# Kernel optimization log

Hardware: AMD Instinct MI355X
Metric: run time of the kernel (lower is better)

Reference implementation:

```python
import jax, jax.numpy as jnp
import numpy as np

# dims: L blocks, S cur_seq, M memory_len, B batch, D embed, H heads, IN input_dim
L, S, M, B, D, H, IN = 4, 512, 512, 8, 1024, 16, 128
HD = D // H
GRU_BIAS = 2.0  # config['gru_bias']


def _ln(x, s, b, eps=1e-5):
    mu = x.mean(-1, keepdims=True)
    var = ((x - mu) ** 2).mean(-1, keepdims=True)
    return (x - mu) * jax.lax.rsqrt(var + eps) * s + b


def _pos_emb(full_seq, dim):
    # SinusoidalPE: freqs = arange(0, dim, 2.0); inv = 10000**(-freqs/dim); seq descending
    freqs = jnp.arange(0, dim, 2.0)
    inv = 10000.0 ** (-freqs / dim)
    seq = jnp.arange(full_seq - 1, -1, -1.0)
    ang = seq[:, None] * inv[None, :]
    return jnp.concatenate([jnp.sin(ang), jnp.cos(ang)], axis=-1)  # (F, dim)


def _rel_shift(x):
    # x: (q, k, b, h) -> Transformer-XL relative shift
    q, k, b, h = x.shape
    xp = jnp.pad(x, ((0, 0), (1, 0), (0, 0), (0, 0)))
    return xp.reshape(k + 1, q, b, h)[1:].reshape(q, k, b, h)


def _gru(x, y, Wr, Ur, Wz, Uz, Wg, Ug):
    r = jax.nn.sigmoid(y @ Wr + x @ Ur)
    z = jax.nn.sigmoid(y @ Wz + x @ Uz - GRU_BIAS)
    hcand = jnp.tanh(y @ Wg + (r * x) @ Ug)
    return (1.0 - z) * x + z * hcand


def setup_inputs() -> dict:
    key = jax.random.key(0)
    ks = iter(jax.random.split(key, 64))

    def mat(*shape):
        return jax.random.normal(next(ks), shape, jnp.float32) * (shape[-2] ** -0.5)

    return dict(
        h=jax.random.normal(next(ks), (B, S, IN), jnp.float32),
        memory=jnp.zeros((L, M, B, D), jnp.float32),
        We=mat(IN, D), be=jnp.zeros((D,), jnp.float32),
        ln1_s=jnp.ones((L, D), jnp.float32), ln1_b=jnp.zeros((L, D), jnp.float32),
        ln2_s=jnp.ones((L, D), jnp.float32), ln2_b=jnp.zeros((L, D), jnp.float32),
        Wq=mat(L, D, D), bq=jnp.zeros((L, D), jnp.float32),
        Wk=mat(L, D, D), bk=jnp.zeros((L, D), jnp.float32),
        Wv=mat(L, D, D), bv=jnp.zeros((L, D), jnp.float32),
        Wr=mat(L, D, D), br=jnp.zeros((L, D), jnp.float32),
        Wo=mat(L, D, D), bo=jnp.zeros((L, D), jnp.float32),
        u=jax.random.normal(next(ks), (L, H, HD), jnp.float32) * 0.02,
        vb=jax.random.normal(next(ks), (L, H, HD), jnp.float32) * 0.02,
        gWr=mat(L, 2, D, D), gUr=mat(L, 2, D, D),
        gWz=mat(L, 2, D, D), gUz=mat(L, 2, D, D),
        gWg=mat(L, 2, D, D), gUg=mat(L, 2, D, D),
        fW1=mat(L, D, 4 * D), fb1=jnp.zeros((L, 4 * D), jnp.float32),
        fW2=mat(L, 4 * D, D), fb2=jnp.zeros((L, D), jnp.float32),
    )


def reference(h, memory, We, be, ln1_s, ln1_b, ln2_s, ln2_b,
              Wq, bq, Wk, bk, Wv, bv, Wr, br, Wo, bo, u, vb,
              gWr, gUr, gWz, gUz, gWg, gUg, fW1, fb1, fW2, fb2):
    x = jnp.transpose(h, (1, 0, 2))                      # (S, B, IN)
    x = jax.nn.gelu(x @ We + be, approximate=False)      # (S, B, D)
    F = S + M
    pos = _pos_emb(F, D)                                 # (F, D)
    mask = jnp.triu(jnp.ones((S, F), bool), k=1 + M)     # (S, F)
    scale = HD ** -0.5
    out = x
    for i in range(L):
        full = jnp.concatenate([memory[i], out], axis=0)  # (F, B, D)
        qn = _ln(out, ln1_s[i], ln1_b[i])
        kn = _ln(full, ln1_s[i], ln1_b[i])
        q = (qn @ Wq[i] + bq[i]).reshape(S, B, H, HD)
        k = (kn @ Wk[i] + bk[i]).reshape(F, B, H, HD)
        v = (kn @ Wv[i] + bv[i]).reshape(F, B, H, HD)
        r = (pos @ Wr[i] + br[i]).reshape(F, H, HD)
        content = jnp.einsum('ibhd,jbhd->ijbh', q + u[i], k)
        position = _rel_shift(jnp.einsum('ibhd,jhd->ijbh', q + vb[i], r))
        attn = (content + position) * scale               # (S, F, B, H)
        attn = jnp.where(mask[:, :, None, None], -1e30, attn)
        a = jax.nn.softmax(attn, axis=1)
        y = jnp.einsum('ijbh,jbhd->ibhd', a, v).reshape(S, B, D) @ Wo[i] + bo[i]
        y = jax.nn.gelu(y, approximate=False)
        out1 = _gru(out, y, gWr[i, 0], gUr[i, 0], gWz[i, 0], gUz[i, 0], gWg[i, 0], gUg[i, 0])
        e = _ln(out1, ln2_s[i], ln2_b[i])
        e = jax.nn.gelu(e @ fW1[i] + fb1[i], approximate=False)
        e = jax.nn.gelu(e @ fW2[i] + fb2[i], approximate=False)
        out = _gru(out1, e, gWr[i, 1], gUr[i, 1], gWz[i, 1], gUz[i, 1], gWg[i, 1], gUg[i, 1])
    return jnp.transpose(out, (1, 0, 2))                  # (B, S, D)
```

## Files before the change

### kernel.cpp

```cpp
#include <hip/hip_runtime.h>

typedef unsigned short u16;
typedef unsigned long long u64;
typedef __attribute__((ext_vector_type(8))) short bf16x8;
typedef __attribute__((ext_vector_type(4))) float f32x4;

#define DEVI __device__ __forceinline__

DEVI u16 f2b(float f) {
  unsigned u = __float_as_uint(f);
  u += 0x7fffu + ((u >> 16) & 1u);
  return (u16)(u >> 16);
}
DEVI float b2f(u16 v) { return __uint_as_float((unsigned)v << 16); }
DEVI float tanh_f(float x) {
  float xc = fminf(fmaxf(x, -15.f), 15.f);
  float e = __expf(2.f * xc);
  return (e - 1.f) / (e + 1.f);
}
DEVI float gelu_f(float x) {
  float u = 0.7978845608028654f * x * (1.f + 0.044715f * x * x);
  return 0.5f * x * (1.f + tanh_f(u));
}
DEVI float sigm_f(float x) { return 1.f / (1.f + __expf(-x)); }

DEVI void gload16(const void* g, void* l) {
  __builtin_amdgcn_global_load_lds((__attribute__((address_space(1))) void*)g,
                                   (__attribute__((address_space(3))) void*)l, 16, 0, 0);
}

template <int BN>
__global__ __launch_bounds__(256) void gemm_bt(
    const u16* __restrict__ A, const u16* __restrict__ Bt,
    const float* __restrict__ bias, const float* __restrict__ bias2,
    float* __restrict__ C32, u16* __restrict__ C16, u16* __restrict__ C16b,
    int M, int N, int K, int ldA, int ldB, int ldC,
    long long sA, long long sBb, long long sBh, long long sC, int nH, int flags)
{
  constexpr int NF = BN / 32;
  __shared__ __align__(16) u16 Sm[2][(128 + BN) * 64];
  const int z = blockIdx.z;
  const int zb = z / nH, zh = z - zb * nH;
  A  += (long long)z * sA;
  Bt += (long long)zb * sBb + (long long)zh * sBh;
  const long long cOff = (long long)z * sC;
  const int m0 = blockIdx.x * 128, n0 = blockIdx.y * BN;
  const int t = threadIdx.x, lane = t & 63;
  const int wm = ((t >> 7) & 1) * 64, wn = ((t >> 6) & 1) * (BN / 2);

  f32x4 acc[4][NF];
#pragma unroll
  for (int i = 0; i < 4; ++i)
#pragma unroll
    for (int j = 0; j < NF; ++j) { f32x4 zz = {0.f, 0.f, 0.f, 0.f}; acc[i][j] = zz; }

  auto stage = [&](int buf, int k0) {
#pragma unroll
    for (int r = 0; r < 4; ++r) {
      const int c = r * 256 + t;
      const int row = c >> 3;
      const int col = (c & 7) << 3;
      int ga = m0 + row; if (ga >= M) ga = M - 1;
      gload16(A + (long long)ga * ldA + (k0 + col),
              &Sm[buf][(size_t)(r * 256 + (t & 192)) * 8]);
    }
#pragma unroll
    for (int r = 0; r < BN / 32; ++r) {
      const int c = r * 256 + t;
      const int row = c >> 3;
      const int col = (c & 7) << 3;
      int gb = n0 + row; if (gb >= N) gb = N - 1;
      gload16(Bt + (long long)gb * ldB + (k0 + col),
              &Sm[buf][(size_t)(1024 + r * 256 + (t & 192)) * 8]);
    }
  };

  auto compute = [&](int buf) {
    const u16* As = &Sm[buf][0];
    const u16* Bs = &Sm[buf][128 * 64];
#pragma unroll
    for (int ks = 0; ks < 2; ++ks) {
      const int ko = ks * 32 + ((lane >> 4) << 3);
      bf16x8 af[4], bfv[NF];
#pragma unroll
      for (int i = 0; i < 4; ++i)
        af[i] = *(const bf16x8*)&As[(wm + i * 16 + (lane & 15)) * 64 + ko];
#pragma unroll
      for (int i = 0; i < NF; ++i)
        bfv[i] = *(const bf16x8*)&Bs[(wn + i * 16 + (lane & 15)) * 64 + ko];
#pragma unroll
      for (int mi = 0; mi < 4; ++mi)
#pragma unroll
        for (int ni = 0; ni < NF; ++ni)
          acc[mi][ni] = __builtin_amdgcn_mfma_f32_16x16x32_bf16(af[mi], bfv[ni], acc[mi][ni], 0, 0, 0);
    }
  };

  stage(0, 0);
  __syncthreads();
  int cur = 0;
  for (int k0 = 64; k0 < K; k0 += 64) {
    stage(cur ^ 1, k0);
    compute(cur);
    __syncthreads();
    cur ^= 1;
  }
  compute(cur);

  const int cb = n0 + wn + (lane & 15);
  const int rb = m0 + wm + ((lane >> 4) << 2);
#pragma unroll
  for (int ni = 0; ni < NF; ++ni) {
    const int col = cb + ni * 16;
    if (col >= N) continue;
    float bv = 0.f;
    if (flags & 2) bv = ((flags & 128) && zh) ? bias2[col] : bias[col];
#pragma unroll
    for (int mi = 0; mi < 4; ++mi) {
#pragma unroll
      for (int q = 0; q < 4; ++q) {
        const int row = rb + mi * 16 + q;
        if (row >= M) continue;
        float x = acc[mi][ni][q] + bv;
        if (flags & 1) x = gelu_f(x);
        if (flags & 64) {
          const long long o = ((long long)((row & 7) * 16 + (col >> 6)) * ldC + (row >> 3)) * 64 + (col & 63);
          C16[o] = f2b(x);
          C16b[o] = f2b(x + bias2[col]);
        } else if (flags & 128) {
          if (zh == 0) {
            const long long o = ((long long)((row & 7) * 16 + (col >> 6)) * ldC + (row >> 3)) * 64 + (col & 63);
            C16[o] = f2b(x);
          } else {
            C16b[(long long)row * 1024 + col] = f2b(x);
          }
        } else {
          long long o;
          if (flags & 16)
            o = ((long long)((row & 7) * 16 + (col >> 6)) * ldC + (row >> 3)) * 64 + (col & 63);
          else if (flags & 32)
            o = ((long long)(col >> 6) * 1024 + row) * 64 + (col & 63);
          else
            o = cOff + (long long)row * ldC + col;
          if (flags & 4) C32[o] = x;
          if (flags & 8) C16[o] = f2b(x);
        }
      }
    }
  }
}

__global__ __launch_bounds__(256) void fused_attn(
    const u16* __restrict__ Qu,
    const u16* __restrict__ Qv,
    const u16* __restrict__ Kb,
    const u16* __restrict__ Vt,
    const u16* __restrict__ Rh,
    u16* __restrict__ Y)
{
  constexpr int F = 1024;
  constexpr float KSC = 0.1803368801111244f;
  const int bid = blockIdx.x;
  const int wk = (bid & 7) * 128 + (bid >> 3);
  const int i0 = (wk & 7) * 64;
  const int bh = wk >> 3;
  const int h = bh & 15;

  __shared__ __align__(16) u16 Ks[2][64 * 64];
  __shared__ __align__(16) u16 Vs[2][64 * 64];
  __shared__ __align__(16) u16 Rs[2][64 * 64];
  __shared__ __align__(8) u16 PBT[2][64 * 68];
  __shared__ __align__(16) u16 Ps[4][16][72];

  const int t = threadIdx.x;
  const int lane = t & 63;
  const int wq = t >> 6;
  const int l15 = lane & 15, lhi = lane >> 4;

  const u16* QUg = Qu + ((size_t)bh * 512 + i0) * 64;
  const u16* QVg = Qv + ((size_t)bh * 512 + i0) * 64;
  const u16* Kg = Kb + (size_t)bh * F * 64;
  const u16* Vg = Vt + (size_t)bh * 64 * F;
  const u16* Rg = Rh + (size_t)h * F * 64;

  bf16x8 au[2], av[2];
#pragma unroll
  for (int ks = 0; ks < 2; ++ks) {
    const int arow = wq * 16 + l15;
    au[ks] = *(const bf16x8*)(QUg + arow * 64 + ks * 32 + lhi * 8);
    av[ks] = *(const bf16x8*)(QVg + arow * 64 + ks * 32 + lhi * 8);
  }

  auto stageT = [&](const u16* g, u16* dst) {
#pragma unroll
    for (int rnd = 0; rnd < 2; ++rnd) {
      const int idx = rnd * 256 + t;
      const int row = idx >> 3;
      const int gs = (idx & 7) ^ (row & 7);
      gload16(g + row * 64 + gs * 8, dst + (size_t)(rnd * 256 + (t & 192)) * 8);
    }
  };
  auto stageVf = [&](int j0, u16* dst) {
#pragma unroll
    for (int rnd = 0; rnd < 2; ++rnd) {
      const int idx = rnd * 256 + t;
      const int row = idx >> 3;
      const int gs = (idx & 7) ^ (row & 7);
      gload16(Vg + (size_t)row * F + j0 + gs * 8, dst + (size_t)(rnd * 256 + (t & 192)) * 8);
    }
  };

  const int nT = i0 / 64 + 9;

  stageT(Kg, Ks[0]);
  stageVf(0, Vs[0]);
  stageT(Rg + (size_t)(512 - i0) * 64, Rs[0]);
  stageT(Rg + (size_t)(448 - i0) * 64, Rs[1]);
  __syncthreads();
  {
    f32x4 pb0[4];
#pragma unroll
    for (int i = 0; i < 4; ++i) { f32x4 zz = {0.f, 0.f, 0.f, 0.f}; pb0[i] = zz; }
    __builtin_amdgcn_s_setprio(1);
#pragma unroll
    for (int ks = 0; ks < 2; ++ks)
#pragma unroll
      for (int ni = 0; ni < 4; ++ni) {
        const int brow = ni * 16 + l15;
        const bf16x8 br_ = *(const bf16x8*)&Rs[1][brow * 64 + (((ks * 4 + lhi) ^ (brow & 7)) << 3)];
        pb0[ni] = __builtin_amdgcn_mfma_f32_16x16x32_bf16(av[ks], br_, pb0[ni], 0, 0, 0);
      }
    __builtin_amdgcn_s_setprio(0);
#pragma unroll
    for (int ni = 0; ni < 4; ++ni) {
      u64 w = (u64)f2b(pb0[ni][0]) | ((u64)f2b(pb0[ni][1]) << 16) |
              ((u64)f2b(pb0[ni][2]) << 32) | ((u64)f2b(pb0[ni][3]) << 48);
      *(u64*)&PBT[0][(size_t)(ni * 16 + l15) * 68 + wq * 16 + lhi * 4] = w;
    }
  }
  __syncthreads();

  f32x4 Oacc[4];
#pragma unroll
  for (int i = 0; i < 4; ++i) { f32x4 zz = {0.f, 0.f, 0.f, 0.f}; Oacc[i] = zz; }
  float mrow[4] = {-3.0e38f, -3.0e38f, -3.0e38f, -3.0e38f};
  float lrow[4] = {0.f, 0.f, 0.f, 0.f};

  for (int st = 0; st < nT; ++st) {
    const int b = st & 1;
    const bool lastT = (st == nT - 1);

    if (!lastT) {
      const int j1 = (st + 1) * 64;
      stageT(Kg + (size_t)j1 * 64, Ks[b ^ 1]);
      stageVf(j1, Vs[b ^ 1]);
      if (st + 1 < nT - 1)
        stageT(Rg + (size_t)(j1 - i0 + 512) * 64, Rs[b ^ 1]);
    }

    f32x4 cacc[4], pbh[4];
#pragma unroll
    for (int i = 0; i < 4; ++i) {
      f32x4 zz = {0.f, 0.f, 0.f, 0.f};
      cacc[i] = zz; pbh[i] = zz;
    }
    __builtin_amdgcn_s_setprio(1);
#pragma unroll
    for (int ks = 0; ks < 2; ++ks) {
#pragma unroll
      for (int ni = 0; ni < 4; ++ni) {
        const int brow = ni * 16 + l15;
        const bf16x8 bk_ = *(const bf16x8*)&Ks[b][brow * 64 + (((ks * 4 + lhi) ^ (brow & 7)) << 3)];
        cacc[ni] = __builtin_amdgcn_mfma_f32_16x16x32_bf16(au[ks], bk_, cacc[ni], 0, 0, 0);
      }
      if (!lastT) {
#pragma unroll
        for (int ni = 0; ni < 4; ++ni) {
          const int brow = ni * 16 + l15;
          const bf16x8 br_ = *(const bf16x8*)&Rs[b][brow * 64 + (((ks * 4 + lhi) ^ (brow & 7)) << 3)];
          pbh[ni] = __builtin_amdgcn_mfma_f32_16x16x32_bf16(av[ks], br_, pbh[ni], 0, 0, 0);
        }
      }
    }
    __builtin_amdgcn_s_setprio(0);

    if (!lastT) {
#pragma unroll
      for (int ni = 0; ni < 4; ++ni) {
        u64 w = (u64)f2b(pbh[ni][0]) | ((u64)f2b(pbh[ni][1]) << 16) |
                ((u64)f2b(pbh[ni][2]) << 32) | ((u64)f2b(pbh[ni][3]) << 48);
        *(u64*)&PBT[(st + 1) & 1][(size_t)(ni * 16 + l15) * 68 + wq * 16 + lhi * 4] = w;
      }
    }

    const u16* pbLo = &PBT[st & 1][0];
    const u16* pbHi = &PBT[(st + 1) & 1][0];
    float sc[4][4];
#pragma unroll
    for (int ni = 0; ni < 4; ++ni) {
      const int dj = ni * 16 + l15;
#pragma unroll
      for (int qq = 0; qq < 4; ++qq) {
        const int di = wq * 16 + lhi * 4 + qq;
        const int cc = dj - di + 63;
        const float pb = b2f((cc < 64) ? pbLo[(size_t)cc * 68 + di]
                                       : pbHi[(size_t)(cc - 64) * 68 + di]);
        float s = (cacc[ni][qq] + pb) * KSC;
        if (lastT && dj > di) s = -1e30f;
        sc[ni][qq] = s;
      }
    }

    float nm[4], esc[4];
#pragma unroll
    for (int qq = 0; qq < 4; ++qq) {
      float r = fmaxf(fmaxf(sc[0][qq], sc[1][qq]), fmaxf(sc[2][qq], sc[3][qq]));
      r = fmaxf(r, __shfl_xor(r, 1));
      r = fmaxf(r, __shfl_xor(r, 2));
      r = fmaxf(r, __shfl_xor(r, 4));
      r = fmaxf(r, __shfl_xor(r, 8));
      nm[qq] = fmaxf(mrow[qq], r);
      esc[qq] = exp2f(mrow[qq] - nm[qq]);
      mrow[qq] = nm[qq];
    }
    float ps[4][4];
    float rsum[4] = {0.f, 0.f, 0.f, 0.f};
#pragma unroll
    for (int ni = 0; ni < 4; ++ni)
#pragma unroll
      for (int qq = 0; qq < 4; ++qq) {
        float p = exp2f(sc[ni][qq] - nm[qq]);
        ps[ni][qq] = p;
        rsum[qq] += p;
      }
#pragma unroll
    for (int qq = 0; qq < 4; ++qq) {
      float r = rsum[qq];
      r += __shfl_xor(r, 1);
      r += __shfl_xor(r, 2);
      r += __shfl_xor(r, 4);
      r += __shfl_xor(r, 8);
      lrow[qq] = lrow[qq] * esc[qq] + r;
    }
#pragma unroll
    for (int nd = 0; nd < 4; ++nd)
#pragma unroll
      for (int qq = 0; qq < 4; ++qq) Oacc[nd][qq] *= esc[qq];

#pragma unroll
    for (int ni = 0; ni < 4; ++ni)
#pragma unroll
      for (int qq = 0; qq < 4; ++qq)
        Ps[wq][lhi * 4 + qq][ni * 16 + l15] = f2b(ps[ni][qq]);
    __builtin_amdgcn_s_setprio(1);
#pragma unroll
    for (int ks = 0; ks < 2; ++ks) {
      const bf16x8 pa = *(const bf16x8*)&Ps[wq][l15][ks * 32 + lhi * 8];
#pragma unroll
      for (int nd = 0; nd < 4; ++nd) {
        const int vrow = nd * 16 + l15;
        const bf16x8 vb_ = *(const bf16x8*)&Vs[b][vrow * 64 + (((ks * 4 + lhi) ^ (vrow & 7)) << 3)];
        Oacc[nd] = __builtin_amdgcn_mfma_f32_16x16x32_bf16(pa, vb_, Oacc[nd], 0, 0, 0);
      }
    }
    __builtin_amdgcn_s_setprio(0);

    __syncthreads();
  }

  float inv[4];
#pragma unroll
  for (int qq = 0; qq < 4; ++qq) inv[qq] = 1.f / lrow[qq];
  const int b = bh >> 4;
#pragma unroll
  for (int nd = 0; nd < 4; ++nd)
#pragma unroll
    for (int qq = 0; qq < 4; ++qq) {
      const int row = i0 + wq * 16 + lhi * 4 + qq;
      const int d = nd * 16 + l15;
      Y[(size_t)row * 8192 + b * 1024 + h * 64 + d] = f2b(Oacc[nd][qq] * inv[qq]);
    }
}

__global__ __launch_bounds__(256) void biasprep(const float* __restrict__ bq,
                                                const float* __restrict__ u,
                                                const float* __restrict__ vb,
                                                float* __restrict__ bqu,
                                                float* __restrict__ dvb)
{
  const int i = blockIdx.x * 256 + threadIdx.x;
  bqu[i] = bq[i] + u[i];
  dvb[i] = vb[i] - u[i];
}

#define MAXW 20
struct WPack {
  const float* src[MAXW];
  u16* dst[MAXW];
  int K[MAXW], N[MAXW];
  int tilePrefix[MAXW + 1];
  int nm;
};

__global__ __launch_bounds__(256) void wtrans_kernel(WPack p) {
  int bid = blockIdx.x;
  int m = 0;
  while (m < p.nm && bid >= p.tilePrefix[m + 1]) ++m;
  if (m >= p.nm) return;
  const int lt = bid - p.tilePrefix[m];
  const int K = p.K[m], N = p.N[m];
  const int tN = N >> 5;
  const int kt = lt / tN, nt = lt - kt * tN;
  const int k0 = kt << 5, n0 = nt << 5;
  const float* src = p.src[m];
  u16* dst = p.dst[m];
  __shared__ float tile[32][33];
  const int t = threadIdx.x;
  const int r = t >> 3, c4 = (t & 7) << 2;
  float4 v = *(const float4*)&src[(size_t)(k0 + r) * N + n0 + c4];
  tile[r][c4 + 0] = v.x; tile[r][c4 + 1] = v.y; tile[r][c4 + 2] = v.z; tile[r][c4 + 3] = v.w;
  __syncthreads();
  u16 o0 = f2b(tile[c4 + 0][r]);
  u16 o1 = f2b(tile[c4 + 1][r]);
  u16 o2 = f2b(tile[c4 + 2][r]);
  u16 o3 = f2b(tile[c4 + 3][r]);
  u64 w = (u64)o0 | ((u64)o1 << 16) | ((u64)o2 << 32) | ((u64)o3 << 48);
  *(u64*)&dst[(size_t)(n0 + r) * K + k0 + c4] = w;
}

__global__ __launch_bounds__(256) void ln_kernel(
    const float* __restrict__ Xmem, const float* __restrict__ Xout, int rowsMem,
    const float* __restrict__ sc, const float* __restrict__ bi, u16* __restrict__ dst)
{
  const int row = blockIdx.x;
  const float* src = (row < rowsMem) ? (Xmem + (long long)row * 1024)
                                     : (Xout + (long long)(row - rowsMem) * 1024);
  const int t = threadIdx.x;
  float4 v = *(const float4*)&src[t * 4];
  float s1 = v.x + v.y + v.z + v.w;
  float s2 = v.x * v.x + v.y * v.y + v.z * v.z + v.w * v.w;
#pragma unroll
  for (int o = 32; o > 0; o >>= 1) { s1 += __shfl_down(s1, o); s2 += __shfl_down(s2, o); }
  __shared__ float red[8];
  const int wv = t >> 6;
  if ((t & 63) == 0) { red[wv * 2] = s1; red[wv * 2 + 1] = s2; }
  __syncthreads();
  s1 = red[0] + red[2] + red[4] + red[6];
  s2 = red[1] + red[3] + red[5] + red[7];
  const float mu = s1 * (1.f / 1024.f);
  const float var = s2 * (1.f / 1024.f) - mu * mu;
  const float rs = rsqrtf(var + 1e-5f);
  float vals[4] = {v.x, v.y, v.z, v.w};
  u16 o4[4];
#pragma unroll
  for (int j = 0; j < 4; ++j) {
    const int c = t * 4 + j;
    o4[j] = f2b((vals[j] - mu) * rs * sc[c] + bi[c]);
  }
  *(u64*)&dst[(long long)row * 1024 + t * 4] =
      (u64)o4[0] | ((u64)o4[1] << 16) | ((u64)o4[2] << 32) | ((u64)o4[3] << 48);
}

__global__ __launch_bounds__(256) void prep_vt16(const u16* __restrict__ Vf, u16* __restrict__ VT)
{
  const int f0 = blockIdx.x * 64;
  const int bh = blockIdx.y;
  const int b = bh >> 4, h = bh & 15;
  __shared__ u16 tl[64 * 64];
  const int t = threadIdx.x;
  {
    const int fr = t >> 2, c0 = (t & 3) * 16;
    const u16* src = Vf + ((size_t)(f0 + fr) * 8 + b) * 1024 + h * 64 + c0;
    *(bf16x8*)&tl[fr * 64 + c0] = *(const bf16x8*)src;
    *(bf16x8*)&tl[fr * 64 + c0 + 8] = *(const bf16x8*)(src + 8);
  }
  __syncthreads();
  {
    const int dr = t >> 2, c0 = (t & 3) * 16;
    u16* dst = VT + ((long long)bh * 64 + dr) * 1024 + f0 + c0;
#pragma unroll
    for (int j = 0; j < 16; ++j) dst[j] = tl[(c0 + j) * 64 + dr];
  }
}

__global__ __launch_bounds__(256) void pe_kernel(u16* __restrict__ PEB)
{
  const long long idx = (long long)blockIdx.x * 256 + threadIdx.x;
  const int p = (int)(idx >> 10);
  const int d = idx & 1023;
  const int q = d & 511;
  const float inv = powf(10000.f, -(float)(2 * q) * (1.f / 1024.f));
  const float ang = (float)(1023 - p) * inv;
  PEB[idx] = f2b((d < 512) ? sinf(ang) : cosf(ang));
}

__global__ __launch_bounds__(256) void embed_conv(const float* __restrict__ h, u16* __restrict__ A)
{
  const long long idx = (long long)blockIdx.x * 256 + threadIdx.x;
  const int c = idx & 127;
  const int r = (int)(idx >> 7);
  const int s = r >> 3, b = r & 7;
  A[idx] = f2b(h[(((long long)b * 512 + s) << 7) + c]);
}

__global__ __launch_bounds__(256) void gru_elemA(const float* __restrict__ T1, float* __restrict__ T2,
                                                 const float* __restrict__ X, u16* __restrict__ RXBF)
{
  const long long i4 = ((long long)blockIdx.x * 256 + threadIdx.x) * 4;
  const int row = (int)(i4 >> 10);
  const int c = i4 & 1023;
  const float* t1 = T1 + (long long)row * 3072 + c;
  float* t2 = T2 + (long long)row * 2048 + c;
  float4 ry = *(const float4*)t1;
  float4 zy = *(const float4*)(t1 + 1024);
  float4 rx = *(const float4*)t2;
  float4 zx = *(const float4*)(t2 + 1024);
  float4 x = *(const float4*)(X + i4);
  float rr[4], zz[4];
  rr[0] = sigm_f(ry.x + rx.x); rr[1] = sigm_f(ry.y + rx.y);
  rr[2] = sigm_f(ry.z + rx.z); rr[3] = sigm_f(ry.w + rx.w);
  zz[0] = sigm_f(zy.x + zx.x - 2.f); zz[1] = sigm_f(zy.y + zx.y - 2.f);
  zz[2] = sigm_f(zy.z + zx.z - 2.f); zz[3] = sigm_f(zy.w + zx.w - 2.f);
  u16 o4[4];
  o4[0] = f2b(rr[0] * x.x); o4[1] = f2b(rr[1] * x.y);
  o4[2] = f2b(rr[2] * x.z); o4[3] = f2b(rr[3] * x.w);
  *(u64*)&RXBF[i4] = (u64)o4[0] | ((u64)o4[1] << 16) | ((u64)o4[2] << 32) | ((u64)o4[3] << 48);
  float4 zo; zo.x = zz[0]; zo.y = zz[1]; zo.z = zz[2]; zo.w = zz[3];
  *(float4*)t2 = zo;
}

__global__ __launch_bounds__(256) void gru_elemB(const float* __restrict__ T1, const float* __restrict__ T2,
                                                 const float* __restrict__ TG, const float* __restrict__ X,
                                                 float* __restrict__ O, u16* __restrict__ XBF)
{
  const long long i4 = ((long long)blockIdx.x * 256 + threadIdx.x) * 4;
  const int row = (int)(i4 >> 10);
  const int c = i4 & 1023;
  float4 gy = *(const float4*)(T1 + (long long)row * 3072 + 2048 + c);
  float4 tt = *(const float4*)(TG + i4);
  float4 z = *(const float4*)(T2 + (long long)row * 2048 + c);
  float4 x = *(const float4*)(X + i4);
  float4 o;
  o.x = (1.f - z.x) * x.x + z.x * tanh_f(gy.x + tt.x);
  o.y = (1.f - z.y) * x.y + z.y * tanh_f(gy.y + tt.y);
  o.z = (1.f - z.z) * x.z + z.z * tanh_f(gy.z + tt.z);
  o.w = (1.f - z.w) * x.w + z.w * tanh_f(gy.w + tt.w);
  *(float4*)(O + i4) = o;
  u16 o4[4];
  o4[0] = f2b(o.x); o4[1] = f2b(o.y); o4[2] = f2b(o.z); o4[3] = f2b(o.w);
  *(u64*)&XBF[i4] = (u64)o4[0] | ((u64)o4[1] << 16) | ((u64)o4[2] << 32) | ((u64)o4[3] << 48);
}

__global__ __launch_bounds__(256) void out_transpose(const float* __restrict__ O, float* __restrict__ dst)
{
  const long long i4 = ((long long)blockIdx.x * 256 + threadIdx.x) * 4;
  const int d = i4 & 1023;
  const int r = (int)(i4 >> 10);
  const int s = r >> 3, b = r & 7;
  float4 v = *(const float4*)(O + i4);
  *(float4*)&dst[(((long long)b * 512 + s) << 10) + d] = v;
}

extern "C" void kernel_launch(void* const* d_in, const int* in_sizes, int n_in,
                              void* d_out, int out_size, void* d_ws, size_t ws_size,
                              hipStream_t stream)
{
  (void)in_sizes; (void)n_in; (void)out_size; (void)ws_size;
  const float* h_in   = (const float*)d_in[0];
  const float* memory = (const float*)d_in[1];
  const float* We     = (const float*)d_in[2];
  const float* be     = (const float*)d_in[3];
  const float* ln1s   = (const float*)d_in[4];
  const float* ln1b   = (const float*)d_in[5];
  const float* ln2s   = (const float*)d_in[6];
  const float* ln2b   = (const float*)d_in[7];
  const float* Wq     = (const float*)d_in[8];
  const float* bq     = (const float*)d_in[9];
  const float* Wk     = (const float*)d_in[10];
  const float* bk     = (const float*)d_in[11];
  const float* Wv     = (const float*)d_in[12];
  const float* bv     = (const float*)d_in[13];
  const float* Wr     = (const float*)d_in[14];
  const float* br     = (const float*)d_in[15];
  const float* Wo     = (const float*)d_in[16];
  const float* bo     = (const float*)d_in[17];
  const float* uu     = (const float*)d_in[18];
  const float* vbp    = (const float*)d_in[19];
  const float* gWr    = (const float*)d_in[20];
  const float* gUr    = (const float*)d_in[21];
  const float* gWz    = (const float*)d_in[22];
  const float* gUz    = (const float*)d_in[23];
  const float* gWg    = (const float*)d_in[24];
  const float* gUg    = (const float*)d_in[25];
  const float* fW1    = (const float*)d_in[26];
  const float* fb1    = (const float*)d_in[27];
  const float* fW2    = (const float*)d_in[28];
  const float* fb2    = (const float*)d_in[29];

  constexpr int S = 512, MM = 512, B = 8, D = 1024, H = 16, IN = 128, F = 1024;
  constexpr int SB = 4096, FB = 8192;
  constexpr long long DD = (long long)D * D;

  char* ws = (char*)d_ws;
  size_t off = 0;
  auto alloc = [&](size_t bytes) -> size_t {
    size_t o = off; off = (off + bytes + 255) & ~(size_t)255; return o;
  };
  const size_t oWT   = alloc((size_t)25 * DD * 2);
  const size_t oWET  = alloc((size_t)D * IN * 2);
  const size_t oPEB  = alloc((size_t)F * D * 2);
  const size_t oOUT  = alloc((size_t)SB * D * 4);
  const size_t oOUT1 = alloc((size_t)SB * D * 4);
  const size_t oXBF  = alloc((size_t)SB * D * 2);
  const size_t oYBF  = alloc((size_t)SB * D * 2);
  const size_t oYBFA = alloc((size_t)SB * D * 2);
  const size_t oABUF = alloc((size_t)SB * D * 2);
  const size_t oKN   = alloc((size_t)FB * D * 2);
  const size_t oQU   = alloc((size_t)B * H * S * 64 * 2);
  const size_t oQV   = alloc((size_t)B * H * S * 64 * 2);
  const size_t oKBH  = alloc((size_t)B * H * F * 64 * 2);
  const size_t oVT   = alloc((size_t)B * H * F * 64 * 2);
  const size_t oRH   = alloc((size_t)H * F * 64 * 2);
  const size_t oBQU  = alloc((size_t)D * 4);
  const size_t oDVB  = alloc((size_t)D * 4);
  const size_t oUNI  = off;

  u16* WTp   = (u16*)(ws + oWT);
  u16* WETp  = (u16*)(ws + oWET);
  u16* PEBp  = (u16*)(ws + oPEB);
  float* OUTp  = (float*)(ws + oOUT);
  float* OUT1p = (float*)(ws + oOUT1);
  u16* XBFp  = (u16*)(ws + oXBF);
  u16* YBFp  = (u16*)(ws + oYBF);
  u16* YBFAp = (u16*)(ws + oYBFA);
  u16* ABUFp = (u16*)(ws + oABUF);
  u16* KNp   = (u16*)(ws + oKN);
  u16* QUp   = (u16*)(ws + oQU);
  u16* QVp   = (u16*)(ws + oQV);
  u16* KBHp  = (u16*)(ws + oKBH);
  u16* VTp   = (u16*)(ws + oVT);
  u16* RHp   = (u16*)(ws + oRH);
  float* bquP = (float*)(ws + oBQU);
  float* dvbP = (float*)(ws + oDVB);
  u16* VF16p  = (u16*)(ws + oUNI);
  float* T1   = (float*)(ws + oUNI);
  float* T2   = (float*)(ws + oUNI + (size_t)SB * 3 * D * 4);
  float* TGp  = (float*)(ws + oUNI + (size_t)SB * 5 * D * 4);
  u16* FFNBp  = (u16*)(ws + oUNI);

  auto gemm = [&](const u16* A, const u16* Bt, const float* bias, const float* bias2,
                  float* C32, u16* C16, u16* C16b,
                  int M, int N, int K, int ldA, int ldB, int ldC,
                  long long sA, long long sBb, long long sBh, long long sC, int nH, int Z,
                  int flags) {
    if (N <= 1024) {
      dim3 grid((M + 127) / 128, (N + 63) / 64, Z);
      gemm_bt<64><<<grid, 256, 0, stream>>>(A, Bt, bias, bias2, C32, C16, C16b,
                                            M, N, K, ldA, ldB, ldC,
                                            sA, sBb, sBh, sC, nH, flags);
    } else {
      dim3 grid((M + 127) / 128, (N + 127) / 128, Z);
      gemm_bt<128><<<grid, 256, 0, stream>>>(A, Bt, bias, bias2, C32, C16, C16b,
                                             M, N, K, ldA, ldB, ldC,
                                             sA, sBb, sBh, sC, nH, flags);
    }
  };

  pe_kernel<<<(F * D) / 256, 256, 0, stream>>>(PEBp);
  {
    WPack p{};
    p.nm = 1; p.src[0] = We; p.dst[0] = WETp; p.K[0] = IN; p.N[0] = D;
    p.tilePrefix[0] = 0; p.tilePrefix[1] = (IN / 32) * (D / 32);
    wtrans_kernel<<<p.tilePrefix[1], 256, 0, stream>>>(p);
  }
  embed_conv<<<(SB * IN) / 256, 256, 0, stream>>>(h_in, ABUFp);
  gemm(ABUFp, WETp, be, nullptr, OUTp, XBFp, nullptr, SB, D, IN, IN, IN, D,
       0, 0, 0, 0, 1, 1, 1 | 2 | 4 | 8);

  for (int li = 0; li < 4; ++li) {
    WPack p{};
    int nt = 0, id = 0;
    auto addw = [&](const float* s, u16* d, int K, int N) {
      p.src[id] = s; p.dst[id] = d; p.K[id] = K; p.N[id] = N;
      p.tilePrefix[id] = nt; nt += (K / 32) * (N / 32); ++id;
    };
    addw(Wq + li * DD, WTp + 0 * DD, D, D);
    addw(Wk + li * DD, WTp + 1 * DD, D, D);
    addw(Wv + li * DD, WTp + 2 * DD, D, D);
    addw(Wr + li * DD, WTp + 3 * DD, D, D);
    addw(Wo + li * DD, WTp + 4 * DD, D, D);
    addw(gWr + (li * 2 + 0) * DD, WTp + 5 * DD, D, D);
    addw(gWz + (li * 2 + 0) * DD, WTp + 6 * DD, D, D);
    addw(gWg + (li * 2 + 0) * DD, WTp + 7 * DD, D, D);
    addw(gUr + (li * 2 + 0) * DD, WTp + 8 * DD, D, D);
    addw(gUz + (li * 2 + 0) * DD, WTp + 9 * DD, D, D);
    addw(gUg + (li * 2 + 0) * DD, WTp + 10 * DD, D, D);
    addw(gWr + (li * 2 + 1) * DD, WTp + 11 * DD, D, D);
    addw(gWz + (li * 2 + 1) * DD, WTp + 12 * DD, D, D);
    addw(gWg + (li * 2 + 1) * DD, WTp + 13 * DD, D, D);
    addw(gUr + (li * 2 + 1) * DD, WTp + 14 * DD, D, D);
    addw(gUz + (li * 2 + 1) * DD, WTp + 15 * DD, D, D);
    addw(gUg + (li * 2 + 1) * DD, WTp + 16 * DD, D, D);
    addw(fW1 + li * (long long)D * 4096, WTp + 17 * DD, D, 4096);
    addw(fW2 + li * (long long)4096 * D, WTp + 21 * DD, 4096, D);
    p.tilePrefix[id] = nt; p.nm = id;
    wtrans_kernel<<<nt, 256, 0, stream>>>(p);

    ln_kernel<<<FB, 256, 0, stream>>>(memory + (long long)li * MM * B * D, OUTp, MM * B,
                                      ln1s + li * D, ln1b + li * D, KNp);
    const u16* QN = KNp + (size_t)MM * B * D;

    biasprep<<<4, 256, 0, stream>>>(bq + li * D, uu + li * D, vbp + li * D, bquP, dvbP);
    gemm(QN, WTp + 0 * DD, bquP, dvbP, nullptr, QUp, QVp, SB, D, D, D, D,  S,
         0, 0, 0, 0, 1, 1, 2 | 64);
    gemm(KNp, WTp + 1 * DD, bk + li * D, bv + li * D, nullptr, KBHp, VF16p,
         FB, D, D, D, D,  F, 0, 0, DD, 0, 2, 2, 2 | 128);
    prep_vt16<<<dim3(F / 64, B * H), 256, 0, stream>>>(VF16p, VTp);
    gemm(PEBp, WTp + 3 * DD, br + li * D, nullptr, nullptr, RHp, nullptr,
         F, D, D, D, D, D, 0, 0, 0, 0, 1, 1, 2 | 8 | 32);

    fused_attn<<<dim3((S / 64) * B * H), 256, 0, stream>>>(QUp, QVp, KBHp, VTp, RHp, YBFAp);

    gemm(YBFAp, WTp + 4 * DD, bo + li * D, nullptr, nullptr, YBFp, nullptr,
         SB, D, D, D, D, D, 0, 0, 0, 0, 1, 1, 1 | 2 | 8);

    gemm(YBFp, WTp + 5 * DD, nullptr, nullptr, T1, nullptr, nullptr,
         SB, 3 * D, D, D, D, 3 * D, 0, 0, 0, 0, 1, 1, 4);
    gemm(XBFp, WTp + 8 * DD, nullptr, nullptr, T2, nullptr, nullptr,
         SB, 2 * D, D, D, D, 2 * D, 0, 0, 0, 0, 1, 1, 4);
    gru_elemA<<<(SB * D / 4) / 256, 256, 0, stream>>>(T1, T2, OUTp, ABUFp);
    gemm(ABUFp, WTp + 10 * DD, nullptr, nullptr, TGp, nullptr, nullptr,
         SB, D, D, D, D, D, 0, 0, 0, 0, 1, 1, 4);
    gru_elemB<<<(SB * D / 4) / 256, 256, 0, stream>>>(T1, T2, TGp, OUTp, OUT1p, XBFp);

    ln_kernel<<<SB, 256, 0, stream>>>(OUT1p, OUT1p, SB, ln2s + li * D, ln2b + li * D, ABUFp);
    gemm(ABUFp, WTp + 17 * DD, fb1 + li * 4096, nullptr, nullptr, FFNBp, nullptr,
         SB, 4096, D, D, D, 4096, 0, 0, 0, 0, 1, 1, 1 | 2 | 8);
    gemm(FFNBp, WTp + 21 * DD, fb2 + li * D, nullptr, nullptr, YBFp, nullptr,
         SB, D, 4096, 4096, 4096, D, 0, 0, 0, 0, 1, 1, 1 | 2 | 8);

    gemm(YBFp, WTp + 11 * DD, nullptr, nullptr, T1, nullptr, nullptr,
         SB, 3 * D, D, D, D, 3 * D, 0, 0, 0, 0, 1, 1, 4);
    gemm(XBFp, WTp + 14 * DD, nullptr, nullptr, T2, nullptr, nullptr,
         SB, 2 * D, D, D, D, 2 * D, 0, 0, 0, 0, 1, 1, 4);
    gru_elemA<<<(SB * D / 4) / 256, 256, 0, stream>>>(T1, T2, OUT1p, ABUFp);
    gemm(ABUFp, WTp + 16 * DD, nullptr, nullptr, TGp, nullptr, nullptr,
         SB, D, D, D, D, D, 0, 0, 0, 0, 1, 1, 4);
    gru_elemB<<<(SB * D / 4) / 256, 256, 0, stream>>>(T1, T2, TGp, OUT1p, OUTp, XBFp);
  }

  out_transpose<<<(SB * D / 4) / 256, 256, 0, stream>>>(OUTp, (float*)d_out);
}
```

Baseline: 3.289 ms.

## Store GRU GEMM intermediates in bf16 and fold attention scale into Q

The GRU gate GEMMs now write bf16 outputs instead of fp32, and the GRU elementwise kernels read bf16 and process eight elements per thread. This halves the memory traffic of those intermediates. The softmax scale is now applied in the Q projection epilogue instead of per score inside attention, and bf16 packing uses the hardware v_cvt_pk_bf16_f32 instruction. In exchange, the GRU pre-activations and the stored z gate lose precision by being rounded to bf16.

```diff
diff --git a/kernel.cpp b/kernel.cpp
--- a/kernel.cpp
+++ b/kernel.cpp
@@ -7,12 +7,19 @@
 
 #define DEVI __device__ __forceinline__
 
+#define KSC 0.1803368801111244f
+
 DEVI u16 f2b(float f) {
   unsigned u = __float_as_uint(f);
   u += 0x7fffu + ((u >> 16) & 1u);
   return (u16)(u >> 16);
 }
 DEVI float b2f(u16 v) { return __uint_as_float((unsigned)v << 16); }
+DEVI unsigned cvtpk(float lo, float hi) {
+  unsigned r;
+  asm("v_cvt_pk_bf16_f32 %0, %1, %2" : "=v"(r) : "v"(lo), "v"(hi));
+  return r;
+}
 DEVI float tanh_f(float x) {
   float xc = fminf(fmaxf(x, -15.f), 15.f);
   float e = __expf(2.f * xc);
@@ -125,8 +132,8 @@
         if (flags & 1) x = gelu_f(x);
         if (flags & 64) {
           const long long o = ((long long)((row & 7) * 16 + (col >> 6)) * ldC + (row >> 3)) * 64 + (col & 63);
-          C16[o] = f2b(x);
-          C16b[o] = f2b(x + bias2[col]);
+          C16[o] = f2b(x * KSC);
+          C16b[o] = f2b((x + bias2[col]) * KSC);
         } else if (flags & 128) {
           if (zh == 0) {
             const long long o = ((long long)((row & 7) * 16 + (col >> 6)) * ldC + (row >> 3)) * 64 + (col & 63);
@@ -159,7 +166,6 @@
     u16* __restrict__ Y)
 {
   constexpr int F = 1024;
-  constexpr float KSC = 0.1803368801111244f;
   const int bid = blockIdx.x;
   const int wk = (bid & 7) * 128 + (bid >> 3);
   const int i0 = (wk & 7) * 64;
@@ -233,8 +239,7 @@
     __builtin_amdgcn_s_setprio(0);
 #pragma unroll
     for (int ni = 0; ni < 4; ++ni) {
-      u64 w = (u64)f2b(pb0[ni][0]) | ((u64)f2b(pb0[ni][1]) << 16) |
-              ((u64)f2b(pb0[ni][2]) << 32) | ((u64)f2b(pb0[ni][3]) << 48);
+      u64 w = (u64)cvtpk(pb0[ni][0], pb0[ni][1]) | ((u64)cvtpk(pb0[ni][2], pb0[ni][3]) << 32);
       *(u64*)&PBT[0][(size_t)(ni * 16 + l15) * 68 + wq * 16 + lhi * 4] = w;
     }
   }
@@ -287,8 +292,7 @@
     if (!lastT) {
 #pragma unroll
       for (int ni = 0; ni < 4; ++ni) {
-        u64 w = (u64)f2b(pbh[ni][0]) | ((u64)f2b(pbh[ni][1]) << 16) |
-                ((u64)f2b(pbh[ni][2]) << 32) | ((u64)f2b(pbh[ni][3]) << 48);
+        u64 w = (u64)cvtpk(pbh[ni][0], pbh[ni][1]) | ((u64)cvtpk(pbh[ni][2], pbh[ni][3]) << 32);
         *(u64*)&PBT[(st + 1) & 1][(size_t)(ni * 16 + l15) * 68 + wq * 16 + lhi * 4] = w;
       }
     }
@@ -305,7 +309,7 @@
         const int cc = dj - di + 63;
         const float pb = b2f((cc < 64) ? pbLo[(size_t)cc * 68 + di]
                                        : pbHi[(size_t)(cc - 64) * 68 + di]);
-        float s = (cacc[ni][qq] + pb) * KSC;
+        float s = cacc[ni][qq] + pb;
         if (lastT && dj > di) s = -1e30f;
         sc[ni][qq] = s;
       }
@@ -348,10 +352,14 @@
       for (int qq = 0; qq < 4; ++qq) Oacc[nd][qq] *= esc[qq];
 
 #pragma unroll
-    for (int ni = 0; ni < 4; ++ni)
-#pragma unroll
-      for (int qq = 0; qq < 4; ++qq)
-        Ps[wq][lhi * 4 + qq][ni * 16 + l15] = f2b(ps[ni][qq]);
+    for (int ni = 0; ni < 4; ++ni) {
+      unsigned p01 = cvtpk(ps[ni][0], ps[ni][1]);
+      unsigned p23 = cvtpk(ps[ni][2], ps[ni][3]);
+      Ps[wq][lhi * 4 + 0][ni * 16 + l15] = (u16)p01;
+      Ps[wq][lhi * 4 + 1][ni * 16 + l15] = (u16)(p01 >> 16);
+      Ps[wq][lhi * 4 + 2][ni * 16 + l15] = (u16)p23;
+      Ps[wq][lhi * 4 + 3][ni * 16 + l15] = (u16)(p23 >> 16);
+    }
     __builtin_amdgcn_s_setprio(1);
 #pragma unroll
     for (int ks = 0; ks < 2; ++ks) {
@@ -372,14 +380,16 @@
 #pragma unroll
   for (int qq = 0; qq < 4; ++qq) inv[qq] = 1.f / lrow[qq];
   const int b = bh >> 4;
-#pragma unroll
-  for (int nd = 0; nd < 4; ++nd)
-#pragma unroll
-    for (int qq = 0; qq < 4; ++qq) {
-      const int row = i0 + wq * 16 + lhi * 4 + qq;
-      const int d = nd * 16 + l15;
-      Y[(size_t)row * 8192 + b * 1024 + h * 64 + d] = f2b(Oacc[nd][qq] * inv[qq]);
-    }
+  const int rbase = i0 + wq * 16 + lhi * 4;
+#pragma unroll
+  for (int nd = 0; nd < 4; ++nd) {
+    const int d = nd * 16 + l15;
+    unsigned w01 = cvtpk(Oacc[nd][0] * inv[0], Oacc[nd][1] * inv[1]);
+    unsigned w23 = cvtpk(Oacc[nd][2] * inv[2], Oacc[nd][3] * inv[3]);
+    u16* yb = Y + (size_t)rbase * 8192 + b * 1024 + h * 64 + d;
+    yb[0] = (u16)w01; yb[8192] = (u16)(w01 >> 16);
+    yb[16384] = (u16)w23; yb[24576] = (u16)(w23 >> 16);
+  }
 }
 
 __global__ __launch_bounds__(256) void biasprep(const float* __restrict__ bq,
@@ -503,52 +513,63 @@
   A[idx] = f2b(h[(((long long)b * 512 + s) << 7) + c]);
 }
 
-__global__ __launch_bounds__(256) void gru_elemA(const float* __restrict__ T1, float* __restrict__ T2,
+__global__ __launch_bounds__(256) void gru_elemA(const u16* __restrict__ T1, u16* __restrict__ T2,
                                                  const float* __restrict__ X, u16* __restrict__ RXBF)
 {
-  const long long i4 = ((long long)blockIdx.x * 256 + threadIdx.x) * 4;
-  const int row = (int)(i4 >> 10);
-  const int c = i4 & 1023;
-  const float* t1 = T1 + (long long)row * 3072 + c;
-  float* t2 = T2 + (long long)row * 2048 + c;
-  float4 ry = *(const float4*)t1;
-  float4 zy = *(const float4*)(t1 + 1024);
-  float4 rx = *(const float4*)t2;
-  float4 zx = *(const float4*)(t2 + 1024);
-  float4 x = *(const float4*)(X + i4);
-  float rr[4], zz[4];
-  rr[0] = sigm_f(ry.x + rx.x); rr[1] = sigm_f(ry.y + rx.y);
-  rr[2] = sigm_f(ry.z + rx.z); rr[3] = sigm_f(ry.w + rx.w);
-  zz[0] = sigm_f(zy.x + zx.x - 2.f); zz[1] = sigm_f(zy.y + zx.y - 2.f);
-  zz[2] = sigm_f(zy.z + zx.z - 2.f); zz[3] = sigm_f(zy.w + zx.w - 2.f);
-  u16 o4[4];
-  o4[0] = f2b(rr[0] * x.x); o4[1] = f2b(rr[1] * x.y);
-  o4[2] = f2b(rr[2] * x.z); o4[3] = f2b(rr[3] * x.w);
-  *(u64*)&RXBF[i4] = (u64)o4[0] | ((u64)o4[1] << 16) | ((u64)o4[2] << 32) | ((u64)o4[3] << 48);
-  float4 zo; zo.x = zz[0]; zo.y = zz[1]; zo.z = zz[2]; zo.w = zz[3];
-  *(float4*)t2 = zo;
-}
-
-__global__ __launch_bounds__(256) void gru_elemB(const float* __restrict__ T1, const float* __restrict__ T2,
-                                                 const float* __restrict__ TG, const float* __restrict__ X,
+  const long long i8 = ((long long)blockIdx.x * 256 + threadIdx.x) * 8;
+  const int row = (int)(i8 >> 10);
+  const int c = i8 & 1023;
+  const u16* t1 = T1 + (long long)row * 3072 + c;
+  u16* t2 = T2 + (long long)row * 2048 + c;
+  bf16x8 ry = *(const bf16x8*)t1;
+  bf16x8 zy = *(const bf16x8*)(t1 + 1024);
+  bf16x8 rx = *(const bf16x8*)t2;
+  bf16x8 zx = *(const bf16x8*)(t2 + 1024);
+  float4 x0 = *(const float4*)(X + i8);
+  float4 x1 = *(const float4*)(X + i8 + 4);
+  float xs[8] = {x0.x, x0.y, x0.z, x0.w, x1.x, x1.y, x1.z, x1.w};
+  u16 ro[8], zo[8];
+#pragma unroll
+  for (int j = 0; j < 8; ++j) {
+    float r = sigm_f(b2f((u16)ry[j]) + b2f((u16)rx[j]));
+    float z = sigm_f(b2f((u16)zy[j]) + b2f((u16)zx[j]) - 2.f);
+    ro[j] = f2b(r * xs[j]);
+    zo[j] = f2b(z);
+  }
+  *(u64*)&RXBF[i8] = (u64)ro[0] | ((u64)ro[1] << 16) | ((u64)ro[2] << 32) | ((u64)ro[3] << 48);
+  *(u64*)&RXBF[i8 + 4] = (u64)ro[4] | ((u64)ro[5] << 16) | ((u64)ro[6] << 32) | ((u64)ro[7] << 48);
+  *(u64*)&t2[0] = (u64)zo[0] | ((u64)zo[1] << 16) | ((u64)zo[2] << 32) | ((u64)zo[3] << 48);
+  *(u64*)&t2[4] = (u64)zo[4] | ((u64)zo[5] << 16) | ((u64)zo[6] << 32) | ((u64)zo[7] << 48);
+}
+
+__global__ __launch_bounds__(256) void gru_elemB(const u16* __restrict__ T1, const u16* __restrict__ T2,
+                                                 const u16* __restrict__ TG, const float* __restrict__ X,
                                                  float* __restrict__ O, u16* __restrict__ XBF)
 {
-  const long long i4 = ((long long)blockIdx.x * 256 + threadIdx.x) * 4;
-  const int row = (int)(i4 >> 10);
-  const int c = i4 & 1023;
-  float4 gy = *(const float4*)(T1 + (long long)row * 3072 + 2048 + c);
-  float4 tt = *(const float4*)(TG + i4);
-  float4 z = *(const float4*)(T2 + (long long)row * 2048 + c);
-  float4 x = *(const float4*)(X + i4);
-  float4 o;
-  o.x = (1.f - z.x) * x.x + z.x * tanh_f(gy.x + tt.x);
-  o.y = (1.f - z.y) * x.y + z.y * tanh_f(gy.y + tt.y);
-  o.z = (1.f - z.z) * x.z + z.z * tanh_f(gy.z + tt.z);
-  o.w = (1.f - z.w) * x.w + z.w * tanh_f(gy.w + tt.w);
-  *(float4*)(O + i4) = o;
-  u16 o4[4];
-  o4[0] = f2b(o.x); o4[1] = f2b(o.y); o4[2] = f2b(o.z); o4[3] = f2b(o.w);
-  *(u64*)&XBF[i4] = (u64)o4[0] | ((u64)o4[1] << 16) | ((u64)o4[2] << 32) | ((u64)o4[3] << 48);
+  const long long i8 = ((long long)blockIdx.x * 256 + threadIdx.x) * 8;
+  const int row = (int)(i8 >> 10);
+  const int c = i8 & 1023;
+  bf16x8 gy = *(const bf16x8*)(T1 + (long long)row * 3072 + 2048 + c);
+  bf16x8 tt = *(const bf16x8*)(TG + i8);
+  bf16x8 zz = *(const bf16x8*)(T2 + (long long)row * 2048 + c);
+  float4 x0 = *(const float4*)(X + i8);
+  float4 x1 = *(const float4*)(X + i8 + 4);
+  float xs[8] = {x0.x, x0.y, x0.z, x0.w, x1.x, x1.y, x1.z, x1.w};
+  float os[8];
+  u16 ob[8];
+#pragma unroll
+  for (int j = 0; j < 8; ++j) {
+    float z = b2f((u16)zz[j]);
+    float o = (1.f - z) * xs[j] + z * tanh_f(b2f((u16)gy[j]) + b2f((u16)tt[j]));
+    os[j] = o;
+    ob[j] = f2b(o);
+  }
+  float4 o0 = {os[0], os[1], os[2], os[3]};
+  float4 o1 = {os[4], os[5], os[6], os[7]};
+  *(float4*)(O + i8) = o0;
+  *(float4*)(O + i8 + 4) = o1;
+  *(u64*)&XBF[i8] = (u64)ob[0] | ((u64)ob[1] << 16) | ((u64)ob[2] << 32) | ((u64)ob[3] << 48);
+  *(u64*)&XBF[i8 + 4] = (u64)ob[4] | ((u64)ob[5] << 16) | ((u64)ob[6] << 32) | ((u64)ob[7] << 48);
 }
 
 __global__ __launch_bounds__(256) void out_transpose(const float* __restrict__ O, float* __restrict__ dst)
@@ -643,9 +664,9 @@
   float* bquP = (float*)(ws + oBQU);
   float* dvbP = (float*)(ws + oDVB);
   u16* VF16p  = (u16*)(ws + oUNI);
-  float* T1   = (float*)(ws + oUNI);
-  float* T2   = (float*)(ws + oUNI + (size_t)SB * 3 * D * 4);
-  float* TGp  = (float*)(ws + oUNI + (size_t)SB * 5 * D * 4);
+  u16* T1p    = (u16*)(ws + oUNI);
+  u16* T2p    = (u16*)(ws + oUNI + (size_t)SB * 3 * D * 2 + 256);
+  u16* TGp    = (u16*)(ws + oUNI + (size_t)SB * 5 * D * 2 + 512);
   u16* FFNBp  = (u16*)(ws + oUNI);
 
   auto gemm = [&](const u16* A, const u16* Bt, const float* bias, const float* bias2,
@@ -724,14 +745,14 @@
     gemm(YBFAp, WTp + 4 * DD, bo + li * D, nullptr, nullptr, YBFp, nullptr,
          SB, D, D, D, D, D, 0, 0, 0, 0, 1, 1, 1 | 2 | 8);
 
-    gemm(YBFp, WTp + 5 * DD, nullptr, nullptr, T1, nullptr, nullptr,
-         SB, 3 * D, D, D, D, 3 * D, 0, 0, 0, 0, 1, 1, 4);
-    gemm(XBFp, WTp + 8 * DD, nullptr, nullptr, T2, nullptr, nullptr,
-         SB, 2 * D, D, D, D, 2 * D, 0, 0, 0, 0, 1, 1, 4);
-    gru_elemA<<<(SB * D / 4) / 256, 256, 0, stream>>>(T1, T2, OUTp, ABUFp);
-    gemm(ABUFp, WTp + 10 * DD, nullptr, nullptr, TGp, nullptr, nullptr,
-         SB, D, D, D, D, D, 0, 0, 0, 0, 1, 1, 4);
-    gru_elemB<<<(SB * D / 4) / 256, 256, 0, stream>>>(T1, T2, TGp, OUTp, OUT1p, XBFp);
+    gemm(YBFp, WTp + 5 * DD, nullptr, nullptr, nullptr, T1p, nullptr,
+         SB, 3 * D, D, D, D, 3 * D, 0, 0, 0, 0, 1, 1, 8);
+    gemm(XBFp, WTp + 8 * DD, nullptr, nullptr, nullptr, T2p, nullptr,
+         SB, 2 * D, D, D, D, 2 * D, 0, 0, 0, 0, 1, 1, 8);
+    gru_elemA<<<(SB * D / 8) / 256, 256, 0, stream>>>(T1p, T2p, OUTp, ABUFp);
+    gemm(ABUFp, WTp + 10 * DD, nullptr, nullptr, nullptr, TGp, nullptr,
+         SB, D, D, D, D, D, 0, 0, 0, 0, 1, 1, 8);
+    gru_elemB<<<(SB * D / 8) / 256, 256, 0, stream>>>(T1p, T2p, TGp, OUTp, OUT1p, XBFp);
 
     ln_kernel<<<SB, 256, 0, stream>>>(OUT1p, OUT1p, SB, ln2s + li * D, ln2b + li * D, ABUFp);
     gemm(ABUFp, WTp + 17 * DD, fb1 + li * 4096, nullptr, nullptr, FFNBp, nullptr,
@@ -739,14 +760,14 @@
     gemm(FFNBp, WTp + 21 * DD, fb2 + li * D, nullptr, nullptr, YBFp, nullptr,
          SB, D, 4096, 4096, 4096, D, 0, 0, 0, 0, 1, 1, 1 | 2 | 8);
 
-    gemm(YBFp, WTp + 11 * DD, nullptr, nullptr, T1, nullptr, nullptr,
-         SB, 3 * D, D, D, D, 3 * D, 0, 0, 0, 0, 1, 1, 4);
-    gemm(XBFp, WTp + 14 * DD, nullptr, nullptr, T2, nullptr, nullptr,
-         SB, 2 * D, D, D, D, 2 * D, 0, 0, 0, 0, 1, 1, 4);
-    gru_elemA<<<(SB * D / 4) / 256, 256, 0, stream>>>(T1, T2, OUT1p, ABUFp);
-    gemm(ABUFp, WTp + 16 * DD, nullptr, nullptr, TGp, nullptr, nullptr,
-         SB, D, D, D, D, D, 0, 0, 0, 0, 1, 1, 4);
-    gru_elemB<<<(SB * D / 4) / 256, 256, 0, stream>>>(T1, T2, TGp, OUT1p, OUTp, XBFp);
+    gemm(YBFp, WTp + 11 * DD, nullptr, nullptr, nullptr, T1p, nullptr,
+         SB, 3 * D, D, D, D, 3 * D, 0, 0, 0, 0, 1, 1, 8);
+    gemm(XBFp, WTp + 14 * DD, nullptr, nullptr, nullptr, T2p, nullptr,
+         SB, 2 * D, D, D, D, 2 * D, 0, 0, 0, 0, 1, 1, 8);
+    gru_elemA<<<(SB * D / 8) / 256, 256, 0, stream>>>(T1p, T2p, OUT1p, ABUFp);
+    gemm(ABUFp, WTp + 16 * DD, nullptr, nullptr, nullptr, TGp, nullptr,
+         SB, D, D, D, D, D, 0, 0, 0, 0, 1, 1, 8);
+    gru_elemB<<<(SB * D / 8) / 256, 256, 0, stream>>>(T1p, T2p, TGp, OUT1p, OUTp, XBFp);
   }
 
   out_transpose<<<(SB * D / 4) / 256, 256, 0, stream>>>(OUTp, (float*)d_out);
```

Result: faster. 3.145 ms (-4.4%).
